# Optimization experiments

Measured on AMD Instinct MI355X. Metric: run time of the kernel, lower is better.

## Reference

```python
import jax, jax.numpy as jnp
import numpy as np

D_MODEL = 1024
DIM_FF = 4096
N_EXPERTS = 8
TOPK = 2
N_TOKENS = 8192


def setup_inputs() -> dict:
    key = jax.random.key(0)
    ks = jax.random.split(key, 8)
    s_in = 1.0 / np.sqrt(D_MODEL)
    s_ff = 1.0 / np.sqrt(DIM_FF)
    x = jax.random.normal(ks[0], (N_TOKENS, D_MODEL), dtype=jnp.float32)
    Wg = jax.random.uniform(ks[1], (D_MODEL, N_EXPERTS), minval=-s_in, maxval=s_in, dtype=jnp.float32)
    bg = jax.random.uniform(ks[2], (N_EXPERTS,), minval=-s_in, maxval=s_in, dtype=jnp.float32)
    W1 = jax.random.uniform(ks[3], (N_EXPERTS, D_MODEL, DIM_FF), minval=-s_in, maxval=s_in, dtype=jnp.float32)
    b1 = jax.random.uniform(ks[4], (N_EXPERTS, DIM_FF), minval=-s_in, maxval=s_in, dtype=jnp.float32)
    W2 = jax.random.uniform(ks[5], (N_EXPERTS, DIM_FF, D_MODEL), minval=-s_ff, maxval=s_ff, dtype=jnp.float32)
    b2 = jax.random.uniform(ks[6], (N_EXPERTS, D_MODEL), minval=-s_ff, maxval=s_ff, dtype=jnp.float32)
    return {"x": x, "Wg": Wg, "bg": bg, "W1": W1, "b1": b1, "W2": W2, "b2": b2}


def reference(x, Wg, bg, W1, b1, W2, b2):
    # Gate: softmax over experts
    w = jax.nn.softmax(x @ Wg + bg, axis=-1)  # [N, E]
    # Sparse gating: keep top-k, renormalize (matches torch scatter mask)
    _, idx = jax.lax.top_k(w, TOPK)  # [N, K]
    n = w.shape[0]
    mask = jnp.zeros_like(w).at[jnp.arange(n)[:, None], idx].set(1.0)
    w = w * mask
    w = w / (jnp.sum(w, axis=-1, keepdims=True) + 1e-9)
    # Dense per-expert FFN (exact GELU, as torch nn.GELU default)
    h = jax.nn.gelu(jnp.einsum('nd,edf->enf', x, W1) + b1[:, None, :], approximate=False)  # [E,N,F]
    y = jnp.einsum('enf,efd->end', h, W2) + b2[:, None, :]  # [E,N,D]
    out = jnp.einsum('ne,end->nd', w, y)  # weighted combine
    return out
```

## Files before the change

kernel.cpp:

```cpp
#include <hip/hip_runtime.h>
#include <cstdint>

typedef unsigned short u16;
typedef unsigned int u32;

#define N_TOKENS 8192
#define D_MODEL 1024
#define DIM_FF 4096
#define N_EXPERTS 8
#define MAX_SLOTS (N_TOKENS * 2)

typedef __bf16 bf16x8 __attribute__((ext_vector_type(8)));
typedef float f32x4 __attribute__((ext_vector_type(4)));

__device__ __forceinline__ u16 f2bf(float f) {
  u32 u = __float_as_uint(f);
  u32 r = (u + 0x7FFFu + ((u >> 16) & 1u)) >> 16;
  return (u16)r;
}

__device__ __forceinline__ void gl2lds16(const void* g, void* l) {
  __builtin_amdgcn_global_load_lds(
      (__attribute__((address_space(1))) void*)(g),
      (__attribute__((address_space(3))) void*)(l), 16, 0, 0);
}

__global__ __launch_bounds__(256) void gate_kernel(
    const float* __restrict__ x, const float* __restrict__ Wg,
    const float* __restrict__ bg, int* __restrict__ eidx,
    float* __restrict__ ew) {
  int tok = (int)((blockIdx.x * 256 + threadIdx.x) >> 6);
  int lane = threadIdx.x & 63;
  const float* xr = x + (size_t)tok * D_MODEL;
  float acc[8] = {0.f, 0.f, 0.f, 0.f, 0.f, 0.f, 0.f, 0.f};
  for (int j = 0; j < 16; ++j) {
    int d = lane + 64 * j;
    float xv = xr[d];
    float4 wa = *(const float4*)(Wg + d * 8);
    float4 wb = *(const float4*)(Wg + d * 8 + 4);
    acc[0] += xv * wa.x; acc[1] += xv * wa.y; acc[2] += xv * wa.z; acc[3] += xv * wa.w;
    acc[4] += xv * wb.x; acc[5] += xv * wb.y; acc[6] += xv * wb.z; acc[7] += xv * wb.w;
  }
#pragma unroll
  for (int off = 32; off > 0; off >>= 1) {
#pragma unroll
    for (int e = 0; e < 8; ++e) acc[e] += __shfl_xor(acc[e], off, 64);
  }
  if (lane == 0) {
    float p[8], m = -1e30f;
#pragma unroll
    for (int e = 0; e < 8; ++e) { p[e] = acc[e] + bg[e]; m = fmaxf(m, p[e]); }
    float s = 0.f;
#pragma unroll
    for (int e = 0; e < 8; ++e) { p[e] = __expf(p[e] - m); s += p[e]; }
#pragma unroll
    for (int e = 0; e < 8; ++e) p[e] /= s;
    int i0 = 0;
#pragma unroll
    for (int e = 1; e < 8; ++e) if (p[e] > p[i0]) i0 = e;
    int i1 = (i0 == 0) ? 1 : 0;
#pragma unroll
    for (int e = 0; e < 8; ++e) if (e != i0 && p[e] > p[i1]) i1 = e;
    float denom = p[i0] + p[i1] + 1e-9f;
    eidx[2 * tok] = i0; eidx[2 * tok + 1] = i1;
    ew[2 * tok] = p[i0] / denom; ew[2 * tok + 1] = p[i1] / denom;
  }
}

__global__ __launch_bounds__(256) void count_kernel(const int* __restrict__ eidx,
                                                    int* __restrict__ counts) {
  __shared__ int lc[16];
  int tid = threadIdx.x;
  if (tid < 16) lc[tid] = 0;
  __syncthreads();
  int t = blockIdx.x * 256 + tid;
  atomicAdd(&lc[2 * eidx[2 * t]], 1);
  atomicAdd(&lc[2 * eidx[2 * t + 1] + 1], 1);
  __syncthreads();
  if (tid < 16) atomicAdd(&counts[tid], lc[tid]);
}

__global__ void scan_kernel(const int* __restrict__ counts, int* __restrict__ off16) {
  if (threadIdx.x == 0) {
    int o = 0;
    for (int g = 0; g < 16; ++g) { off16[g] = o; o += counts[g]; }
    off16[16] = o;
  }
}

__global__ __launch_bounds__(256) void fill_kernel(
    const int* __restrict__ eidx, const float* __restrict__ ew,
    const int* __restrict__ off16, int* __restrict__ fill,
    int* __restrict__ rowtok, float* __restrict__ rowwt) {
  __shared__ int lc[16];
  __shared__ int lbase[16];
  int tid = threadIdx.x;
  if (tid < 16) lc[tid] = 0;
  __syncthreads();
  int t = blockIdx.x * 256 + tid;
  int e0 = eidx[2 * t], e1 = eidx[2 * t + 1];
  int p0 = atomicAdd(&lc[2 * e0], 1);
  int p1 = atomicAdd(&lc[2 * e1 + 1], 1);
  __syncthreads();
  if (tid < 16) lbase[tid] = atomicAdd(&fill[tid], lc[tid]);
  __syncthreads();
  int pos0 = off16[2 * e0] + lbase[2 * e0] + p0;
  int pos1 = off16[2 * e1 + 1] + lbase[2 * e1 + 1] + p1;
  rowtok[pos0] = t; rowwt[pos0] = ew[2 * t];
  rowtok[pos1] = t; rowwt[pos1] = ew[2 * t + 1];
}

__global__ __launch_bounds__(256) void cvt_x_kernel(const float* __restrict__ in,
                                                    u16* __restrict__ out) {
  size_t t = (size_t)blockIdx.x * 256 + threadIdx.x;
  const float4* ip = (const float4*)in + t * 2;
  float4 a = ip[0], b = ip[1];
  uint4 o;
  o.x = f2bf(a.x) | ((u32)f2bf(a.y) << 16);
  o.y = f2bf(a.z) | ((u32)f2bf(a.w) << 16);
  o.z = f2bf(b.x) | ((u32)f2bf(b.y) << 16);
  o.w = f2bf(b.z) | ((u32)f2bf(b.w) << 16);
  *((uint4*)out + t) = o;
}

__global__ __launch_bounds__(256) void transpose_cvt(const float* __restrict__ in,
                                                     u16* __restrict__ out, int R, int C) {
  int e = blockIdx.z;
  const float* ip = in + (size_t)e * R * C;
  u16* op = out + (size_t)e * R * C;
  int c0 = blockIdx.x * 64, r0 = blockIdx.y * 128;
  __shared__ __align__(16) u16 t[64 * 136];
  int tid = threadIdx.x;
  int j4 = (tid & 15) * 4;
#pragma unroll
  for (int p = 0; p < 8; ++p) {
    int i = (tid >> 4) + 16 * p;
    float4 v = *(const float4*)(ip + (size_t)(r0 + i) * C + c0 + j4);
    t[(j4 + 0) * 136 + i] = f2bf(v.x);
    t[(j4 + 1) * 136 + i] = f2bf(v.y);
    t[(j4 + 2) * 136 + i] = f2bf(v.z);
    t[(j4 + 3) * 136 + i] = f2bf(v.w);
  }
  __syncthreads();
  int i8 = (tid & 15) * 8;
#pragma unroll
  for (int p = 0; p < 4; ++p) {
    int c = (tid >> 4) + 16 * p;
    uint4 val = *(const uint4*)&t[c * 136 + i8];
    *(uint4*)(op + (size_t)(c0 + c) * R + r0 + i8) = val;
  }
}

__global__ __launch_bounds__(256) void fc1_kernel(
    const u16* __restrict__ xb, const u16* __restrict__ w1t,
    const float* __restrict__ b1, const int* __restrict__ rowtok,
    const int* __restrict__ off16, u16* __restrict__ H) {
  const int b = blockIdx.x;
  const int e = b & 7;
  const int lin = b >> 3;
  const int rt = lin & 63;
  const int ct = lin >> 6;
  const int base = off16[2 * e];
  const int count = off16[2 * e + 2] - base;
  if (rt * 128 >= count) return;

  __shared__ __align__(16) __bf16 As[128 * 32];
  __shared__ __align__(16) __bf16 Bs[128 * 32];

  const int tid = threadIdx.x;
  const int lane = tid & 63;
  const int wave = tid >> 6;

  const int ra = tid >> 2;
  const int lastslot = base + count - 1;
  int s0 = base + rt * 128 + ra;       if (s0 > lastslot) s0 = lastslot;
  int s1 = base + rt * 128 + ra + 64;  if (s1 > lastslot) s1 = lastslot;
  const size_t koff = (size_t)(tid & 3) * 8;
  const u16* ga0 = xb + (size_t)rowtok[s0] * D_MODEL + koff;
  const u16* ga1 = xb + (size_t)rowtok[s1] * D_MODEL + koff;
  const u16* gb0 = w1t + (size_t)e * DIM_FF * D_MODEL + (size_t)(ct * 128 + ra) * D_MODEL + koff;
  const u16* gb1 = gb0 + (size_t)64 * D_MODEL;

  __bf16* lA0 = As + tid * 8;
  __bf16* lA1 = As + (tid + 256) * 8;
  __bf16* lB0 = Bs + tid * 8;
  __bf16* lB1 = Bs + (tid + 256) * 8;

  const int wm = (wave & 1) * 64;
  const int wn = (wave >> 1) * 64;
  const int quad = lane >> 4;
  const int lc = lane & 15;
  const __bf16* Ap = As + (wm + lc) * 32 + quad * 8;
  const __bf16* Bp = Bs + (wn + lc) * 32 + quad * 8;

  f32x4 acc[4][4];
#pragma unroll
  for (int i = 0; i < 4; ++i)
#pragma unroll
    for (int j = 0; j < 4; ++j) acc[i][j] = (f32x4)0.0f;

  for (int kt = 0; kt < D_MODEL / 32; ++kt) {
    gl2lds16(ga0 + kt * 32, lA0);
    gl2lds16(ga1 + kt * 32, lA1);
    gl2lds16(gb0 + kt * 32, lB0);
    gl2lds16(gb1 + kt * 32, lB1);
    __syncthreads();
    bf16x8 af[4], bfr[4];
#pragma unroll
    for (int mi = 0; mi < 4; ++mi) af[mi] = *(const bf16x8*)(Ap + mi * 16 * 32);
#pragma unroll
    for (int ni = 0; ni < 4; ++ni) bfr[ni] = *(const bf16x8*)(Bp + ni * 16 * 32);
#pragma unroll
    for (int mi = 0; mi < 4; ++mi)
#pragma unroll
      for (int ni = 0; ni < 4; ++ni)
        acc[mi][ni] = __builtin_amdgcn_mfma_f32_16x16x32_bf16(af[mi], bfr[ni], acc[mi][ni], 0, 0, 0);
    __syncthreads();
  }

  float bias[4];
#pragma unroll
  for (int ni = 0; ni < 4; ++ni) bias[ni] = b1[e * DIM_FF + ct * 128 + wn + ni * 16 + lc];
#pragma unroll
  for (int mi = 0; mi < 4; ++mi) {
#pragma unroll
    for (int r = 0; r < 4; ++r) {
      int m = wm + mi * 16 + quad * 4 + r;
      int grow = rt * 128 + m;
      if (grow < count) {
        size_t rowbase = (size_t)(base + grow) * DIM_FF + ct * 128 + wn;
#pragma unroll
        for (int ni = 0; ni < 4; ++ni) {
          float v = acc[mi][ni][r] + bias[ni];
          float t3 = v * (1.0f + 0.044715f * v * v);
          float u = __builtin_amdgcn_exp2f(fminf(2.302208f * t3, 80.0f));
          float h = v * u * __builtin_amdgcn_rcpf(u + 1.0f);
          H[rowbase + ni * 16 + lc] = f2bf(h);
        }
      }
    }
  }
}

__global__ __launch_bounds__(256) void fc2_kernel(
    const u16* __restrict__ H, const u16* __restrict__ w2t,
    const float* __restrict__ b2, const int* __restrict__ rowtok,
    const float* __restrict__ rowwt, const int* __restrict__ off16,
    float* __restrict__ out, int kpass) {
  const int b = blockIdx.x;
  const int e = b & 7;
  const int lin = b >> 3;
  const int rt = lin & 63;
  const int ct = lin >> 6;
  const int base = off16[2 * e + kpass];
  const int cnt  = off16[2 * e + kpass + 1] - base;
  if (rt * 128 >= cnt) return;

  __shared__ __align__(16) __bf16 As[128 * 32];
  __shared__ __align__(16) __bf16 Bs[128 * 32];

  const int tid = threadIdx.x;
  const int lane = tid & 63;
  const int wave = tid >> 6;

  const int ra = tid >> 2;
  const size_t koff = (size_t)(tid & 3) * 8;
  const u16* ga0 = H + (size_t)(base + rt * 128 + ra) * DIM_FF + koff;
  const u16* ga1 = ga0 + (size_t)64 * DIM_FF;
  const u16* gb0 = w2t + (size_t)e * D_MODEL * DIM_FF + (size_t)(ct * 128 + ra) * DIM_FF + koff;
  const u16* gb1 = gb0 + (size_t)64 * DIM_FF;

  __bf16* lA0 = As + tid * 8;
  __bf16* lA1 = As + (tid + 256) * 8;
  __bf16* lB0 = Bs + tid * 8;
  __bf16* lB1 = Bs + (tid + 256) * 8;

  const int wm = (wave & 1) * 64;
  const int wn = (wave >> 1) * 64;
  const int quad = lane >> 4;
  const int lc = lane & 15;
  const __bf16* Ap = As + (wm + lc) * 32 + quad * 8;
  const __bf16* Bp = Bs + (wn + lc) * 32 + quad * 8;

  f32x4 acc[4][4];
#pragma unroll
  for (int i = 0; i < 4; ++i)
#pragma unroll
    for (int j = 0; j < 4; ++j) acc[i][j] = (f32x4)0.0f;

  for (int kt = 0; kt < DIM_FF / 32; ++kt) {
    gl2lds16(ga0 + kt * 32, lA0);
    gl2lds16(ga1 + kt * 32, lA1);
    gl2lds16(gb0 + kt * 32, lB0);
    gl2lds16(gb1 + kt * 32, lB1);
    __syncthreads();
    bf16x8 af[4], bfr[4];
#pragma unroll
    for (int mi = 0; mi < 4; ++mi) af[mi] = *(const bf16x8*)(Ap + mi * 16 * 32);
#pragma unroll
    for (int ni = 0; ni < 4; ++ni) bfr[ni] = *(const bf16x8*)(Bp + ni * 16 * 32);
#pragma unroll
    for (int mi = 0; mi < 4; ++mi)
#pragma unroll
      for (int ni = 0; ni < 4; ++ni)
        acc[mi][ni] = __builtin_amdgcn_mfma_f32_16x16x32_bf16(af[mi], bfr[ni], acc[mi][ni], 0, 0, 0);
    __syncthreads();
  }

  float bias[4];
#pragma unroll
  for (int ni = 0; ni < 4; ++ni) bias[ni] = b2[e * D_MODEL + ct * 128 + wn + ni * 16 + lc];

#pragma unroll
  for (int mi = 0; mi < 4; ++mi) {
#pragma unroll
    for (int r = 0; r < 4; ++r) {
      int m = wm + mi * 16 + quad * 4 + r;
      int grow = rt * 128 + m;
      if (grow < cnt) {
        int slot = base + grow;
        float wt = rowwt[slot];
        float* orow = out + (size_t)rowtok[slot] * D_MODEL + ct * 128 + wn;
        if (kpass == 0) {
#pragma unroll
          for (int ni = 0; ni < 4; ++ni)
            orow[ni * 16 + lc] = wt * (acc[mi][ni][r] + bias[ni]);
        } else {
#pragma unroll
          for (int ni = 0; ni < 4; ++ni)
            orow[ni * 16 + lc] += wt * (acc[mi][ni][r] + bias[ni]);
        }
      }
    }
  }
}

extern "C" void kernel_launch(void* const* d_in, const int* in_sizes, int n_in,
                              void* d_out, int out_size, void* d_ws, size_t ws_size,
                              hipStream_t stream) {
  (void)in_sizes; (void)n_in; (void)ws_size; (void)out_size;
  const float* x  = (const float*)d_in[0];
  const float* Wg = (const float*)d_in[1];
  const float* bg = (const float*)d_in[2];
  const float* W1 = (const float*)d_in[3];
  const float* b1 = (const float*)d_in[4];
  const float* W2 = (const float*)d_in[5];
  const float* b2 = (const float*)d_in[6];
  float* out = (float*)d_out;

  char* ws = (char*)d_ws;
  size_t off = 0;
  int*   counts  = (int*)(ws + 0);
  int*   fill    = (int*)(ws + 128);
  int*   off16   = (int*)(ws + 256);
  off = 4096;
  int*   eidx    = (int*)(ws + off); off += 65536;
  float* ew      = (float*)(ws + off); off += 65536;
  int*   rowtok  = (int*)(ws + off); off += 65536;
  float* rowwt   = (float*)(ws + off); off += 65536;
  u16*   xb      = (u16*)(ws + off); off += (size_t)N_TOKENS * D_MODEL * 2;
  u16*   w1t     = (u16*)(ws + off);
  u16*   w2t     = w1t;
  off += (size_t)N_EXPERTS * DIM_FF * D_MODEL * 2;
  u16*   H       = (u16*)(ws + off);
  off += (size_t)(MAX_SLOTS + 128) * DIM_FF * 2;

  hipMemsetAsync(ws, 0, 4096, stream);

  gate_kernel<<<N_TOKENS / 4, 256, 0, stream>>>(x, Wg, bg, eidx, ew);
  count_kernel<<<N_TOKENS / 256, 256, 0, stream>>>(eidx, counts);
  scan_kernel<<<1, 64, 0, stream>>>(counts, off16);
  fill_kernel<<<N_TOKENS / 256, 256, 0, stream>>>(eidx, ew, off16, fill, rowtok, rowwt);
  cvt_x_kernel<<<(N_TOKENS * D_MODEL / 8) / 256, 256, 0, stream>>>(x, xb);
  transpose_cvt<<<dim3(DIM_FF / 64, D_MODEL / 128, N_EXPERTS), 256, 0, stream>>>(W1, w1t, D_MODEL, DIM_FF);
  fc1_kernel<<<N_EXPERTS * (DIM_FF / 128) * 64, 256, 0, stream>>>(xb, w1t, b1, rowtok, off16, H);
  transpose_cvt<<<dim3(D_MODEL / 64, DIM_FF / 128, N_EXPERTS), 256, 0, stream>>>(W2, w2t, DIM_FF, D_MODEL);
  fc2_kernel<<<N_EXPERTS * (D_MODEL / 128) * 64, 256, 0, stream>>>(H, w2t, b2, rowtok, rowwt, off16, out, 0);
  fc2_kernel<<<N_EXPERTS * (D_MODEL / 128) * 64, 256, 0, stream>>>(H, w2t, b2, rowtok, rowwt, off16, out, 1);
}
```

Before: 781.5 us.

## Fuse x bf16 conversion into gate, drop scan kernel, rework weight transpose

The gate kernel now reads x as float2 and writes the bf16 copy of x itself, so the separate cvt_x pass over x is removed. The scan kernel is dropped: fill_kernel computes prefix offsets in shared memory, and the fc1/fc2 kernels recompute their base offsets from counts. The weight transpose-convert uses 64x64 tiles, packed bf16 LDS writes and paired-column output stores. Together these cut kernel launches and one full read of x, at the cost of redundant per-block prefix sums and a different LDS access pattern in the transpose.

```diff
diff --git a/kernel.cpp b/kernel.cpp
--- a/kernel.cpp
+++ b/kernel.cpp
@@ -18,6 +18,10 @@
   u32 r = (u + 0x7FFFu + ((u >> 16) & 1u)) >> 16;
   return (u16)r;
 }
+__device__ __forceinline__ u16 bfc(float f) {
+  __bf16 b = (__bf16)f;
+  return __builtin_bit_cast(u16, b);
+}
 
 __device__ __forceinline__ void gl2lds16(const void* g, void* l) {
   __builtin_amdgcn_global_load_lds(
@@ -28,18 +32,30 @@
 __global__ __launch_bounds__(256) void gate_kernel(
     const float* __restrict__ x, const float* __restrict__ Wg,
     const float* __restrict__ bg, int* __restrict__ eidx,
-    float* __restrict__ ew) {
+    float* __restrict__ ew, u16* __restrict__ xb) {
   int tok = (int)((blockIdx.x * 256 + threadIdx.x) >> 6);
   int lane = threadIdx.x & 63;
   const float* xr = x + (size_t)tok * D_MODEL;
+  u16* xbr = xb + (size_t)tok * D_MODEL;
   float acc[8] = {0.f, 0.f, 0.f, 0.f, 0.f, 0.f, 0.f, 0.f};
-  for (int j = 0; j < 16; ++j) {
-    int d = lane + 64 * j;
-    float xv = xr[d];
-    float4 wa = *(const float4*)(Wg + d * 8);
-    float4 wb = *(const float4*)(Wg + d * 8 + 4);
-    acc[0] += xv * wa.x; acc[1] += xv * wa.y; acc[2] += xv * wa.z; acc[3] += xv * wa.w;
-    acc[4] += xv * wb.x; acc[5] += xv * wb.y; acc[6] += xv * wb.z; acc[7] += xv * wb.w;
+#pragma unroll
+  for (int j = 0; j < 8; ++j) {
+    int d = 2 * lane + 128 * j;
+    float2 xv = *(const float2*)(xr + d);
+    float4 wa0 = *(const float4*)(Wg + d * 8);
+    float4 wb0 = *(const float4*)(Wg + d * 8 + 4);
+    float4 wa1 = *(const float4*)(Wg + d * 8 + 8);
+    float4 wb1 = *(const float4*)(Wg + d * 8 + 12);
+    acc[0] += xv.x * wa0.x + xv.y * wa1.x;
+    acc[1] += xv.x * wa0.y + xv.y * wa1.y;
+    acc[2] += xv.x * wa0.z + xv.y * wa1.z;
+    acc[3] += xv.x * wa0.w + xv.y * wa1.w;
+    acc[4] += xv.x * wb0.x + xv.y * wb1.x;
+    acc[5] += xv.x * wb0.y + xv.y * wb1.y;
+    acc[6] += xv.x * wb0.z + xv.y * wb1.z;
+    acc[7] += xv.x * wb0.w + xv.y * wb1.w;
+    u32 pk = (u32)f2bf(xv.x) | ((u32)f2bf(xv.y) << 16);
+    *(u32*)(xbr + d) = pk;
   }
 #pragma unroll
   for (int off = 32; off > 0; off >>= 1) {
@@ -80,20 +96,13 @@
   if (tid < 16) atomicAdd(&counts[tid], lc[tid]);
 }
 
-__global__ void scan_kernel(const int* __restrict__ counts, int* __restrict__ off16) {
-  if (threadIdx.x == 0) {
-    int o = 0;
-    for (int g = 0; g < 16; ++g) { off16[g] = o; o += counts[g]; }
-    off16[16] = o;
-  }
-}
-
 __global__ __launch_bounds__(256) void fill_kernel(
     const int* __restrict__ eidx, const float* __restrict__ ew,
-    const int* __restrict__ off16, int* __restrict__ fill,
+    const int* __restrict__ counts, int* __restrict__ fill,
     int* __restrict__ rowtok, float* __restrict__ rowwt) {
   __shared__ int lc[16];
   __shared__ int lbase[16];
+  __shared__ int loff[16];
   int tid = threadIdx.x;
   if (tid < 16) lc[tid] = 0;
   __syncthreads();
@@ -103,24 +112,15 @@
   int p1 = atomicAdd(&lc[2 * e1 + 1], 1);
   __syncthreads();
   if (tid < 16) lbase[tid] = atomicAdd(&fill[tid], lc[tid]);
-  __syncthreads();
-  int pos0 = off16[2 * e0] + lbase[2 * e0] + p0;
-  int pos1 = off16[2 * e1 + 1] + lbase[2 * e1 + 1] + p1;
+  if (tid == 64) {
+    int o = 0;
+    for (int g = 0; g < 16; ++g) { loff[g] = o; o += counts[g]; }
+  }
+  __syncthreads();
+  int pos0 = loff[2 * e0] + lbase[2 * e0] + p0;
+  int pos1 = loff[2 * e1 + 1] + lbase[2 * e1 + 1] + p1;
   rowtok[pos0] = t; rowwt[pos0] = ew[2 * t];
   rowtok[pos1] = t; rowwt[pos1] = ew[2 * t + 1];
-}
-
-__global__ __launch_bounds__(256) void cvt_x_kernel(const float* __restrict__ in,
-                                                    u16* __restrict__ out) {
-  size_t t = (size_t)blockIdx.x * 256 + threadIdx.x;
-  const float4* ip = (const float4*)in + t * 2;
-  float4 a = ip[0], b = ip[1];
-  uint4 o;
-  o.x = f2bf(a.x) | ((u32)f2bf(a.y) << 16);
-  o.y = f2bf(a.z) | ((u32)f2bf(a.w) << 16);
-  o.z = f2bf(b.x) | ((u32)f2bf(b.y) << 16);
-  o.w = f2bf(b.z) | ((u32)f2bf(b.w) << 16);
-  *((uint4*)out + t) = o;
 }
 
 __global__ __launch_bounds__(256) void transpose_cvt(const float* __restrict__ in,
@@ -128,40 +128,52 @@
   int e = blockIdx.z;
   const float* ip = in + (size_t)e * R * C;
   u16* op = out + (size_t)e * R * C;
-  int c0 = blockIdx.x * 64, r0 = blockIdx.y * 128;
-  __shared__ __align__(16) u16 t[64 * 136];
+  int c0 = blockIdx.x * 64, r0 = blockIdx.y * 64;
+  __shared__ __align__(16) u16 t[64 * 68];
   int tid = threadIdx.x;
-  int j4 = (tid & 15) * 4;
-#pragma unroll
-  for (int p = 0; p < 8; ++p) {
-    int i = (tid >> 4) + 16 * p;
-    float4 v = *(const float4*)(ip + (size_t)(r0 + i) * C + c0 + j4);
-    t[(j4 + 0) * 136 + i] = f2bf(v.x);
-    t[(j4 + 1) * 136 + i] = f2bf(v.y);
-    t[(j4 + 2) * 136 + i] = f2bf(v.z);
-    t[(j4 + 3) * 136 + i] = f2bf(v.w);
-  }
-  __syncthreads();
-  int i8 = (tid & 15) * 8;
+  int c4 = (tid & 15) * 4;
 #pragma unroll
   for (int p = 0; p < 4; ++p) {
-    int c = (tid >> 4) + 16 * p;
-    uint4 val = *(const uint4*)&t[c * 136 + i8];
-    *(uint4*)(op + (size_t)(c0 + c) * R + r0 + i8) = val;
-  }
+    int r = (tid >> 4) + 16 * p;
+    float4 v = *(const float4*)(ip + (size_t)(r0 + r) * C + c0 + c4);
+    uint2 pk;
+    pk.x = (u32)bfc(v.x) | ((u32)bfc(v.y) << 16);
+    pk.y = (u32)bfc(v.z) | ((u32)bfc(v.w) << 16);
+    *(uint2*)&t[r * 68 + c4] = pk;
+  }
+  __syncthreads();
+  int pair = tid >> 3;
+  int r8 = (tid & 7) * 8;
+  int c = 2 * pair;
+  u32 u[8];
+#pragma unroll
+  for (int j = 0; j < 8; ++j) u[j] = *(const u32*)&t[(r8 + j) * 68 + c];
+  uint4 lo, hi;
+  lo.x = (u[0] & 0xffffu) | (u[1] << 16);
+  lo.y = (u[2] & 0xffffu) | (u[3] << 16);
+  lo.z = (u[4] & 0xffffu) | (u[5] << 16);
+  lo.w = (u[6] & 0xffffu) | (u[7] << 16);
+  hi.x = (u[0] >> 16) | (u[1] & 0xffff0000u);
+  hi.y = (u[2] >> 16) | (u[3] & 0xffff0000u);
+  hi.z = (u[4] >> 16) | (u[5] & 0xffff0000u);
+  hi.w = (u[6] >> 16) | (u[7] & 0xffff0000u);
+  *(uint4*)(op + (size_t)(c0 + c) * R + r0 + r8) = lo;
+  *(uint4*)(op + (size_t)(c0 + c + 1) * R + r0 + r8) = hi;
 }
 
 __global__ __launch_bounds__(256) void fc1_kernel(
     const u16* __restrict__ xb, const u16* __restrict__ w1t,
     const float* __restrict__ b1, const int* __restrict__ rowtok,
-    const int* __restrict__ off16, u16* __restrict__ H) {
+    const int* __restrict__ counts, u16* __restrict__ H) {
   const int b = blockIdx.x;
   const int e = b & 7;
   const int lin = b >> 3;
   const int rt = lin & 63;
   const int ct = lin >> 6;
-  const int base = off16[2 * e];
-  const int count = off16[2 * e + 2] - base;
+  int base = 0;
+#pragma unroll
+  for (int g = 0; g < 16; ++g) base += (g < 2 * e) ? counts[g] : 0;
+  const int count = counts[2 * e] + counts[2 * e + 1];
   if (rt * 128 >= count) return;
 
   __shared__ __align__(16) __bf16 As[128 * 32];
@@ -245,15 +257,17 @@
 __global__ __launch_bounds__(256) void fc2_kernel(
     const u16* __restrict__ H, const u16* __restrict__ w2t,
     const float* __restrict__ b2, const int* __restrict__ rowtok,
-    const float* __restrict__ rowwt, const int* __restrict__ off16,
+    const float* __restrict__ rowwt, const int* __restrict__ counts,
     float* __restrict__ out, int kpass) {
   const int b = blockIdx.x;
   const int e = b & 7;
   const int lin = b >> 3;
   const int rt = lin & 63;
   const int ct = lin >> 6;
-  const int base = off16[2 * e + kpass];
-  const int cnt  = off16[2 * e + kpass + 1] - base;
+  int base = 0;
+#pragma unroll
+  for (int g = 0; g < 16; ++g) base += (g < 2 * e + kpass) ? counts[g] : 0;
+  const int cnt = counts[2 * e + kpass];
   if (rt * 128 >= cnt) return;
 
   __shared__ __align__(16) __bf16 As[128 * 32];
@@ -352,7 +366,6 @@
   size_t off = 0;
   int*   counts  = (int*)(ws + 0);
   int*   fill    = (int*)(ws + 128);
-  int*   off16   = (int*)(ws + 256);
   off = 4096;
   int*   eidx    = (int*)(ws + off); off += 65536;
   float* ew      = (float*)(ws + off); off += 65536;
@@ -367,14 +380,12 @@
 
   hipMemsetAsync(ws, 0, 4096, stream);
 
-  gate_kernel<<<N_TOKENS / 4, 256, 0, stream>>>(x, Wg, bg, eidx, ew);
+  gate_kernel<<<N_TOKENS / 4, 256, 0, stream>>>(x, Wg, bg, eidx, ew, xb);
   count_kernel<<<N_TOKENS / 256, 256, 0, stream>>>(eidx, counts);
-  scan_kernel<<<1, 64, 0, stream>>>(counts, off16);
-  fill_kernel<<<N_TOKENS / 256, 256, 0, stream>>>(eidx, ew, off16, fill, rowtok, rowwt);
-  cvt_x_kernel<<<(N_TOKENS * D_MODEL / 8) / 256, 256, 0, stream>>>(x, xb);
-  transpose_cvt<<<dim3(DIM_FF / 64, D_MODEL / 128, N_EXPERTS), 256, 0, stream>>>(W1, w1t, D_MODEL, DIM_FF);
-  fc1_kernel<<<N_EXPERTS * (DIM_FF / 128) * 64, 256, 0, stream>>>(xb, w1t, b1, rowtok, off16, H);
-  transpose_cvt<<<dim3(D_MODEL / 64, DIM_FF / 128, N_EXPERTS), 256, 0, stream>>>(W2, w2t, DIM_FF, D_MODEL);
-  fc2_kernel<<<N_EXPERTS * (D_MODEL / 128) * 64, 256, 0, stream>>>(H, w2t, b2, rowtok, rowwt, off16, out, 0);
-  fc2_kernel<<<N_EXPERTS * (D_MODEL / 128) * 64, 256, 0, stream>>>(H, w2t, b2, rowtok, rowwt, off16, out, 1);
-}
+  fill_kernel<<<N_TOKENS / 256, 256, 0, stream>>>(eidx, ew, counts, fill, rowtok, rowwt);
+  transpose_cvt<<<dim3(DIM_FF / 64, D_MODEL / 64, N_EXPERTS), 256, 0, stream>>>(W1, w1t, D_MODEL, DIM_FF);
+  fc1_kernel<<<N_EXPERTS * (DIM_FF / 128) * 64, 256, 0, stream>>>(xb, w1t, b1, rowtok, counts, H);
+  transpose_cvt<<<dim3(D_MODEL / 64, DIM_FF / 64, N_EXPERTS), 256, 0, stream>>>(W2, w2t, DIM_FF, D_MODEL);
+  fc2_kernel<<<N_EXPERTS * (D_MODEL / 128) * 64, 256, 0, stream>>>(H, w2t, b2, rowtok, rowwt, counts, out, 0);
+  fc2_kernel<<<N_EXPERTS * (D_MODEL / 128) * 64, 256, 0, stream>>>(H, w2t, b2, rowtok, rowwt, counts, out, 1);
+}
```

New measurement: 775.8 us. No clear change (-0.7%).
